# Kernel tuning notes

Measured on AMD Instinct MI355X. Metric: run time of the kernel, lower is better.

## Reference

```python
import jax, jax.numpy as jnp
import numpy as np

DIM = 96
D_STATE = 16
D_CONV = 4
EXPAND = 2
D_INNER = EXPAND * DIM          # 192
DT_RANK = (DIM + 15) // 16      # 6
B, DD, HH, WW = 2, 20, 20, 20
LN_EPS = 1e-5


def setup_inputs() -> dict:
    key = jax.random.key(0)
    ks = jax.random.split(key, 10)
    s = 0.02
    x = jax.random.normal(ks[0], (B, DIM, DD, HH, WW), jnp.float32)
    principal_vector = jax.random.normal(ks[1], (3,), jnp.float32)
    norm_w = jnp.ones((DIM,), jnp.float32)
    norm_b = jnp.zeros((DIM,), jnp.float32)
    in_proj_w = jax.random.normal(ks[2], (2 * D_INNER, DIM), jnp.float32) * s
    conv_w = jax.random.normal(ks[3], (D_INNER, 1, D_CONV), jnp.float32) * 0.3  # depthwise kernel (OIH)
    conv_b = jnp.zeros((D_INNER,), jnp.float32)
    x_proj_w = jax.random.normal(ks[4], (DT_RANK + 2 * D_STATE, D_INNER), jnp.float32) * s
    dt_proj_w = jax.random.normal(ks[5], (D_INNER, DT_RANK), jnp.float32) * (DT_RANK ** -0.5)
    dt_proj_b = jnp.full((D_INNER,), float(np.log(np.expm1(0.01))), jnp.float32)  # softplus^-1(0.01)
    # S4D-real init: A = [1..d_state] per inner channel
    A_log = jnp.log(jnp.broadcast_to(jnp.arange(1, D_STATE + 1, dtype=jnp.float32), (D_INNER, D_STATE)))
    D_param = jnp.ones((D_INNER,), jnp.float32)
    out_proj_w = jax.random.normal(ks[6], (DIM, D_INNER), jnp.float32) * s
    return {"x": x, "principal_vector": principal_vector, "norm_w": norm_w, "norm_b": norm_b,
            "in_proj_w": in_proj_w, "conv_w": conv_w, "conv_b": conv_b, "x_proj_w": x_proj_w,
            "dt_proj_w": dt_proj_w, "dt_proj_b": dt_proj_b, "A_log": A_log, "D_param": D_param,
            "out_proj_w": out_proj_w}


def _mamba(xn, in_proj_w, conv_w, conv_b, x_proj_w, dt_proj_w, dt_proj_b, A_log, D_param, out_proj_w):
    # xn: (B, N, dim)
    xz = jnp.einsum('bnc,ec->bne', xn, in_proj_w)          # (B,N,2*d_inner), no bias
    xc, z = jnp.split(xz, 2, axis=-1)
    # causal depthwise conv1d over sequence, truncated to length N
    xc_t = xc.transpose(0, 2, 1)                           # (B, d_inner, N)
    xc_t = jax.lax.conv_general_dilated(
        xc_t, conv_w, window_strides=(1,), padding=[(D_CONV - 1, 0)],
        dimension_numbers=('NCH', 'OIH', 'NCH'), feature_group_count=D_INNER)
    xc = jax.nn.silu(xc_t + conv_b[None, :, None]).transpose(0, 2, 1)  # (B,N,d_inner)
    x_dbl = jnp.einsum('bnd,ed->bne', xc, x_proj_w)
    dt, Bm, Cm = jnp.split(x_dbl, [DT_RANK, DT_RANK + D_STATE], axis=-1)
    dt = jax.nn.softplus(jnp.einsum('bnr,dr->bnd', dt, dt_proj_w) + dt_proj_b)  # (B,N,d_inner)
    A = -jnp.exp(A_log)                                    # (d_inner, d_state)
    dA = jnp.exp(dt[..., None] * A)                        # (B,N,d_inner,d_state)
    dBx = dt[..., None] * Bm[:, :, None, :] * xc[..., None]

    def comb(c1, c2):
        a1, b1 = c1
        a2, b2 = c2
        return (a1 * a2, a2 * b1 + b2)

    _, h = jax.lax.associative_scan(comb, (dA, dBx), axis=1)  # h_t = dA_t*h_{t-1}+dBx_t
    y = jnp.einsum('bnds,bns->bnd', h, Cm) + D_param * xc
    y = y * jax.nn.silu(z)
    return jnp.einsum('bnd,cd->bnc', y, out_proj_w)


def reference(x, principal_vector, norm_w, norm_b, in_proj_w, conv_w, conv_b, x_proj_w,
              dt_proj_w, dt_proj_b, A_log, D_param, out_proj_w):
    Bb, C, D_, H_, W_ = x.shape
    N = D_ * H_ * W_
    zz, yy, xx = jnp.meshgrid(jnp.arange(D_), jnp.arange(H_), jnp.arange(W_), indexing='ij')
    coords = jnp.stack([zz, yy, xx], axis=-1).reshape(-1, 3).astype(jnp.float32)
    projections = coords @ principal_vector
    sorted_idx = jnp.argsort(projections)
    inv_idx = jnp.argsort(sorted_idx)                      # inverse permutation for scatter-back
    x_flat = x.reshape(Bb, C, N)[:, :, sorted_idx].transpose(0, 2, 1)  # (B,N,C) in PCA order
    mu = x_flat.mean(axis=-1, keepdims=True)
    var = x_flat.var(axis=-1, keepdims=True)               # biased, as torch LayerNorm
    xn = (x_flat - mu) / jnp.sqrt(var + LN_EPS) * norm_w + norm_b
    y = _mamba(xn, in_proj_w, conv_w, conv_b, x_proj_w, dt_proj_w, dt_proj_b, A_log, D_param, out_proj_w)
    out = y[:, inv_idx, :]                                 # back to raster order
    return out.transpose(0, 2, 1).reshape(Bb, C, D_, H_, W_)
```

## Files before the change

### kernel.cpp

```cpp
#include <hip/hip_runtime.h>
#include <math.h>

#define NB 2
#define NC 96
#define NN 8000
#define DI 192
#define DS 16
#define DTRK 6
#define KCH 320
#define LCH 25

#define OFF_RP   0
#define OFF_XN   64000
#define OFF_XC   (OFF_XN + NB*NN*NC)
#define OFF_Z    (OFF_XC + NB*NN*DI)
#define OFF_XCV  (OFF_Z  + NB*NN*DI)
#define OFF_DT   (OFF_XCV + NB*NN*DI)
#define OFF_BM   (OFF_DT + NB*NN*DI)
#define OFF_CM   (OFF_BM + NB*NN*DS)
#define OFF_CA   (OFF_CM + NB*NN*DS)
#define OFF_CB   (OFF_CA + NB*KCH*DI*DS)
#define OFF_HS   (OFF_CB + NB*KCH*DI*DS)
#define OFF_Y    (OFF_HS + NB*KCH*DI*DS)
#define OFF_YP   (OFF_Y  + NB*NN*DI)

__global__ void k_rank(const float* __restrict__ pv, int* __restrict__ rp) {
    __shared__ float kj[1000];
    int t = threadIdx.x;
    float p0 = pv[0], p1 = pv[1], p2 = pv[2];
    int j0 = blockIdx.y * 1000;
    for (int j = t; j < 1000; j += 256) {
        int idx = j0 + j;
        int zz = idx / 400, rem = idx % 400, yy = rem / 20, xx = rem % 20;
        kj[j] = (float)zz * p0 + (float)yy * p1 + (float)xx * p2;
    }
    __syncthreads();
    int i = blockIdx.x * 256 + t;
    if (i >= NN) return;
    {
        int zz = i / 400, rem = i % 400, yy = rem / 20, xx = rem % 20;
        float ki = (float)zz * p0 + (float)yy * p1 + (float)xx * p2;
        int cnt = 0;
        #pragma unroll 4
        for (int j = 0; j < 1000; ++j) {
            float kv = kj[j];
            int jj = j0 + j;
            cnt += (kv < ki || (kv == ki && jj < i)) ? 1 : 0;
        }
        rp[blockIdx.y * 8000 + i] = cnt;
    }
}

__launch_bounds__(256)
__global__ void k_ln(const float* __restrict__ x, const float* __restrict__ nw,
                     const float* __restrict__ nbp, const int* __restrict__ rp,
                     float* __restrict__ xn) {
    __shared__ float xt[64][100];
    __shared__ int rk[64];
    __shared__ float nwb[NC], nbb[NC];
    int b = blockIdx.y, n0 = blockIdx.x * 64, t = threadIdx.x;
    int lane = t & 63, w = t >> 6;
    if (t < 64) {
        int s = 0;
        #pragma unroll
        for (int c = 0; c < 8; ++c) s += rp[c * 8000 + n0 + t];
        rk[t] = s;
    } else if (t >= 64 && t < 160) { int c = t - 64; nwb[c] = nw[c]; nbb[c] = nbp[c]; }
    for (int idx = t; idx < NC * 64; idx += 256) {
        int c = idx >> 6, p = idx & 63;
        xt[p][c] = x[((size_t)b * NC + c) * NN + n0 + p];
    }
    __syncthreads();
    float xr[96];
    float s = 0.f, sq = 0.f;
    #pragma unroll
    for (int c4 = 0; c4 < 24; ++c4) {
        float4 v = *(const float4*)&xt[lane][c4 * 4];
        xr[c4*4+0] = v.x; xr[c4*4+1] = v.y; xr[c4*4+2] = v.z; xr[c4*4+3] = v.w;
        s += v.x + v.y + v.z + v.w;
        sq += v.x*v.x + v.y*v.y + v.z*v.z + v.w*v.w;
    }
    float mu = s * (1.f / 96.f);
    float var = sq * (1.f / 96.f) - mu * mu;
    float rs = rsqrtf(var + 1e-5f);
    #pragma unroll
    for (int c = 0; c < 96; ++c) xr[c] = (xr[c] - mu) * rs * nwb[c] + nbb[c];
    __syncthreads();
    if (w == 0) {
        #pragma unroll
        for (int c = 0; c < 96; ++c) xt[lane][c] = xr[c];
    }
    __syncthreads();
    for (int idx = t; idx < 64 * 24; idx += 256) {
        int p = idx / 24, c4 = idx % 24;
        *(float4*)&xn[((size_t)b * NN + rk[p]) * NC + c4 * 4] = *(const float4*)&xt[p][c4 * 4];
    }
}

__launch_bounds__(256, 3)
__global__ void k_inproj(const float* __restrict__ xn, const float* __restrict__ win,
                         float* __restrict__ xcout, float* __restrict__ zout) {
    __shared__ float wsm[48][100];
    __shared__ float xs[64][100];
    int b = blockIdx.z, g = blockIdx.y, n0 = blockIdx.x * 64, t = threadIdx.x;

    for (int i = t; i < 48 * 24; i += 256) {
        int r = i / 24, c4 = i % 24;
        *(float4*)&wsm[r][c4 * 4] = *(const float4*)(win + (size_t)(g * 48 + r) * NC + c4 * 4);
    }
    for (int i = t; i < 64 * 24; i += 256) {
        int p = i / 24, c4 = i % 24;
        *(float4*)&xs[p][c4 * 4] = *(const float4*)(xn + ((size_t)b * NN + n0 + p) * NC + c4 * 4);
    }
    __syncthreads();

    int oi = t & 15, pi = t >> 4;
    float acc[3][4];
    #pragma unroll
    for (int j = 0; j < 3; ++j)
        #pragma unroll
        for (int pp = 0; pp < 4; ++pp) acc[j][pp] = 0.f;

    for (int c4 = 0; c4 < 24; ++c4) {
        float4 b0 = *(const float4*)&wsm[oi * 3 + 0][c4 * 4];
        float4 b1 = *(const float4*)&wsm[oi * 3 + 1][c4 * 4];
        float4 b2 = *(const float4*)&wsm[oi * 3 + 2][c4 * 4];
        #pragma unroll
        for (int pp = 0; pp < 4; ++pp) {
            float4 a = *(const float4*)&xs[pi * 4 + pp][c4 * 4];
            acc[0][pp] = fmaf(a.x, b0.x, fmaf(a.y, b0.y, fmaf(a.z, b0.z, fmaf(a.w, b0.w, acc[0][pp]))));
            acc[1][pp] = fmaf(a.x, b1.x, fmaf(a.y, b1.y, fmaf(a.z, b1.z, fmaf(a.w, b1.w, acc[1][pp]))));
            acc[2][pp] = fmaf(a.x, b2.x, fmaf(a.y, b2.y, fmaf(a.z, b2.z, fmaf(a.w, b2.w, acc[2][pp]))));
        }
    }
    __syncthreads();
    #pragma unroll
    for (int j = 0; j < 3; ++j)
        #pragma unroll
        for (int pp = 0; pp < 4; ++pp) xs[pi * 4 + pp][oi * 3 + j] = acc[j][pp];
    __syncthreads();

    float* outp = (g < 4) ? xcout : zout;
    int co = (g & 3) * 48;
    for (int i = t; i < 64 * 12; i += 256) {
        int p = i / 12, o4 = i % 12;
        *(float4*)&outp[((size_t)b * NN + n0 + p) * DI + co + o4 * 4] = *(const float4*)&xs[p][o4 * 4];
    }
}

__launch_bounds__(256, 8)
__global__ void k_conv_xdt(const float* __restrict__ cw, const float* __restrict__ cb,
                           const float* __restrict__ xpw, const float* __restrict__ dpw,
                           const float* __restrict__ dpb, const float* __restrict__ xcin,
                           float* __restrict__ xcvout, float* __restrict__ dtout,
                           float* __restrict__ bmout, float* __restrict__ cmout) {
    __shared__ float xcv[8][196];
    __shared__ float dtrT[DTRK][9];
    __shared__ float bc[8][33];
    __shared__ float cwT[4][DI];
    __shared__ float dpwT[DTRK][DI];
    __shared__ float cbl[DI], dpbl[DI];
    int b = blockIdx.y, n0 = blockIdx.x * 8, t = threadIdx.x;
    int l = t & 63, w = t >> 6;
    int p = l & 7, q = l >> 3;

    if (t < DI) {
        cbl[t] = cb[t];
        dpbl[t] = dpb[t];
        #pragma unroll
        for (int k = 0; k < 4; ++k) cwT[k][t] = cw[t * 4 + k];
        #pragma unroll
        for (int r = 0; r < DTRK; ++r) dpwT[r][t] = dpw[t * DTRK + r];
    }
    __syncthreads();

    {
        int pp = t / DI, d = t - pp * DI;
        #pragma unroll
        for (int i = 0; i < 6; ++i) {
            float s = cbl[d];
            #pragma unroll
            for (int k = 0; k < 4; ++k) {
                int n = n0 + pp - 3 + k;
                float xv = (n >= 0) ? xcin[((size_t)b * NN + n) * DI + d] : 0.f;
                s = fmaf(cwT[k][d], xv, s);
            }
            s = s * __builtin_amdgcn_rcpf(1.f + __expf(-s));
            xcv[pp][d] = s;
            xcvout[((size_t)b * NN + n0 + pp) * DI + d] = s;
            pp += 1; d += 64;
            if (d >= DI) { d -= DI; pp += 1; }
        }
    }
    __syncthreads();

    float acc[10];
    #pragma unroll
    for (int j = 0; j < 10; ++j) acc[j] = 0.f;
    #pragma unroll
    for (int ci = 0; ci < 6; ++ci) {
        int c4 = q * 6 + ci;
        float4 xv = *(const float4*)&xcv[p][c4 * 4];
        #pragma unroll
        for (int j = 0; j < 10; ++j) {
            int e = w + 4 * j;
            if (e < 38) {
                float4 w4 = *(const float4*)&xpw[(size_t)e * DI + c4 * 4];
                acc[j] = fmaf(xv.x, w4.x, fmaf(xv.y, w4.y, fmaf(xv.z, w4.z, fmaf(xv.w, w4.w, acc[j]))));
            }
        }
    }
    #pragma unroll
    for (int j = 0; j < 10; ++j) {
        acc[j] += __shfl_xor(acc[j], 8);
        acc[j] += __shfl_xor(acc[j], 16);
        acc[j] += __shfl_xor(acc[j], 32);
    }
    if (l < 8) {
        #pragma unroll
        for (int j = 0; j < 10; ++j) {
            int e = w + 4 * j;
            if (e < DTRK) dtrT[e][p] = acc[j];
            else if (e < 38) bc[p][e - DTRK] = acc[j];
        }
    }
    __syncthreads();

    if (t < 8 * DS) {
        int pp = t >> 4, si = t & 15;
        int n = b * NN + n0 + pp;
        bmout[(size_t)n * DS + si] = bc[pp][si];
        cmout[(size_t)n * DS + si] = bc[pp][DS + si];
    }

    float dv[6];
    {
        int d0 = q * 24 + w * 6;
        #pragma unroll
        for (int jd = 0; jd < 6; ++jd) {
            int d = d0 + jd;
            float v = dpbl[d];
            #pragma unroll
            for (int r = 0; r < DTRK; ++r) v = fmaf(dpwT[r][d], dtrT[r][p], v);
            v = (v > 20.f) ? v : __logf(1.f + __expf(v));
            dv[jd] = v;
        }
    }
    __syncthreads();
    {
        int d0 = q * 24 + w * 6;
        #pragma unroll
        for (int jd = 0; jd < 6; ++jd) xcv[p][d0 + jd] = dv[jd];
    }
    __syncthreads();
    for (int idx = t; idx < 8 * 48; idx += 256) {
        int pp = idx / 48, o4 = idx % 48;
        *(float4*)&dtout[((size_t)b * NN + n0 + pp) * DI + o4 * 4] = *(const float4*)&xcv[pp][o4 * 4];
    }
}

__launch_bounds__(256)
__global__ void k_scan1(const float* __restrict__ alog, const float* __restrict__ dt,
                        const float* __restrict__ xcv, const float* __restrict__ bm,
                        float* __restrict__ ca, float* __restrict__ cbv) {
    int t = threadIdx.x, w = t >> 6, l = t & 63;
    int T = blockIdx.x * 4 + w;
    int b = T / (KCH * 6), rem = T % (KCH * 6);
    int kc = rem / 6, dg = rem % 6;
    int dl = l & 31, sh = l >> 5;
    int d = dg * 32 + dl;
    float a[8];
    #pragma unroll
    for (int j = 0; j < 8; ++j) a[j] = -expf(alog[d * DS + sh * 8 + j]);
    size_t nbase = (size_t)b * NN + kc * LCH;
    float ap[8], hb[8];
    #pragma unroll
    for (int j = 0; j < 8; ++j) { ap[j] = 1.f; hb[j] = 0.f; }
    for (int i = 0; i < LCH; ++i) {
        size_t g = (nbase + i) * DI + d;
        float dtv = dt[g];
        float xv  = xcv[g];
        const float4* b4 = (const float4*)&bm[(nbase + i) * DS + sh * 8];
        float4 b0 = b4[0], b1 = b4[1];
        float bmv[8] = {b0.x,b0.y,b0.z,b0.w,b1.x,b1.y,b1.z,b1.w};
        float bx_ = dtv * xv;
        #pragma unroll
        for (int j = 0; j < 8; ++j) {
            float dA = __expf(dtv * a[j]);
            ap[j] *= dA;
            hb[j] = fmaf(dA, hb[j], bx_ * bmv[j]);
        }
    }
    size_t cidx = ((size_t)(b * KCH + kc) * DI + d) * DS + sh * 8;
    *(float4*)&ca[cidx]      = make_float4(ap[0],ap[1],ap[2],ap[3]);
    *(float4*)&ca[cidx + 4]  = make_float4(ap[4],ap[5],ap[6],ap[7]);
    *(float4*)&cbv[cidx]     = make_float4(hb[0],hb[1],hb[2],hb[3]);
    *(float4*)&cbv[cidx + 4] = make_float4(hb[4],hb[5],hb[6],hb[7]);
}

__global__ void k_scan2(const float* __restrict__ ca, const float* __restrict__ cbv,
                        float* __restrict__ hs) {
    int tid = blockIdx.x * 64 + threadIdx.x;
    int b = tid / (DI * DS), ds_ = tid % (DI * DS);
    size_t base = (size_t)b * KCH * (DI * DS) + ds_;
    float h = 0.f;
    for (int kc = 0; kc < KCH; kc += 8) {
        float av[8], bv[8];
        #pragma unroll
        for (int u = 0; u < 8; ++u) {
            size_t idx = base + (size_t)(kc + u) * (DI * DS);
            av[u] = ca[idx];
            bv[u] = cbv[idx];
        }
        #pragma unroll
        for (int u = 0; u < 8; ++u) {
            hs[base + (size_t)(kc + u) * (DI * DS)] = h;
            h = fmaf(av[u], h, bv[u]);
        }
    }
}

__launch_bounds__(256)
__global__ void k_scan3(const float* __restrict__ alog, const float* __restrict__ Dp,
                        const float* __restrict__ dt, const float* __restrict__ xcv,
                        const float* __restrict__ bm, const float* __restrict__ cm,
                        const float* __restrict__ zin, const float* __restrict__ hs,
                        float* __restrict__ yout) {
    int t = threadIdx.x, w = t >> 6, l = t & 63;
    int T = blockIdx.x * 4 + w;
    int b = T / (KCH * 6), rem = T % (KCH * 6);
    int kc = rem / 6, dg = rem % 6;
    int dl = l & 31, sh = l >> 5;
    int d = dg * 32 + dl;
    float a[8];
    #pragma unroll
    for (int j = 0; j < 8; ++j) a[j] = -expf(alog[d * DS + sh * 8 + j]);
    float dpar = Dp[d];
    size_t nbase = (size_t)b * NN + kc * LCH;
    size_t cidx = ((size_t)(b * KCH + kc) * DI + d) * DS + sh * 8;
    float h[8];
    {
        float4 h0 = *(const float4*)&hs[cidx];
        float4 h1 = *(const float4*)&hs[cidx + 4];
        h[0]=h0.x; h[1]=h0.y; h[2]=h0.z; h[3]=h0.w;
        h[4]=h1.x; h[5]=h1.y; h[6]=h1.z; h[7]=h1.w;
    }
    for (int i = 0; i < LCH; ++i) {
        size_t g = (nbase + i) * DI + d;
        float dtv = dt[g];
        float xv  = xcv[g];
        float zv  = zin[g];
        size_t sb = (nbase + i) * DS + sh * 8;
        const float4* b4 = (const float4*)&bm[sb];
        const float4* c4p = (const float4*)&cm[sb];
        float4 b0 = b4[0], b1 = b4[1];
        float4 c0 = c4p[0], c1 = c4p[1];
        float bmv[8] = {b0.x,b0.y,b0.z,b0.w,b1.x,b1.y,b1.z,b1.w};
        float cmv[8] = {c0.x,c0.y,c0.z,c0.w,c1.x,c1.y,c1.z,c1.w};
        float bx_ = dtv * xv;
        float py = 0.f;
        #pragma unroll
        for (int j = 0; j < 8; ++j) {
            float dA = __expf(dtv * a[j]);
            h[j] = fmaf(dA, h[j], bx_ * bmv[j]);
            py = fmaf(h[j], cmv[j], py);
        }
        py += __shfl_xor(py, 32);
        if (l < 32) {
            float y = py + dpar * xv;
            y *= zv / (1.f + __expf(-zv));
            yout[g] = y;
        }
    }
}

__launch_bounds__(256, 2)
__global__ void k_outproj(const float* __restrict__ ow, const float* __restrict__ yin,
                          float* __restrict__ yp) {
    __shared__ float wsm[32][196];
    __shared__ float yt[64][196];
    int b = blockIdx.z, g = blockIdx.y, n0 = blockIdx.x * 64, t = threadIdx.x;

    for (int i = t; i < 32 * 48; i += 256) {
        int r = i / 48, c4 = i % 48;
        *(float4*)&wsm[r][c4 * 4] = *(const float4*)(ow + (size_t)(g * 32 + r) * DI + c4 * 4);
    }
    for (int i = t; i < 64 * 48; i += 256) {
        int p = i / 48, c4 = i % 48;
        *(float4*)&yt[p][c4 * 4] = *(const float4*)(yin + ((size_t)b * NN + n0 + p) * DI + c4 * 4);
    }
    __syncthreads();

    int l = t & 63, w = t >> 6;
    int oi = l & 7;
    int kq = (l >> 3) & 3;
    int pi = w * 2 + (l >> 5);
    float acc[4][8];
    #pragma unroll
    for (int j = 0; j < 4; ++j)
        #pragma unroll
        for (int pp = 0; pp < 8; ++pp) acc[j][pp] = 0.f;

    for (int c4 = 0; c4 < 12; ++c4) {
        int cg2 = kq * 12 + c4;
        float4 b0 = *(const float4*)&wsm[oi * 4 + 0][cg2 * 4];
        float4 b1 = *(const float4*)&wsm[oi * 4 + 1][cg2 * 4];
        float4 b2 = *(const float4*)&wsm[oi * 4 + 2][cg2 * 4];
        float4 b3 = *(const float4*)&wsm[oi * 4 + 3][cg2 * 4];
        #pragma unroll
        for (int pp = 0; pp < 8; ++pp) {
            float4 a = *(const float4*)&yt[pi * 8 + pp][cg2 * 4];
            acc[0][pp] = fmaf(a.x, b0.x, fmaf(a.y, b0.y, fmaf(a.z, b0.z, fmaf(a.w, b0.w, acc[0][pp]))));
            acc[1][pp] = fmaf(a.x, b1.x, fmaf(a.y, b1.y, fmaf(a.z, b1.z, fmaf(a.w, b1.w, acc[1][pp]))));
            acc[2][pp] = fmaf(a.x, b2.x, fmaf(a.y, b2.y, fmaf(a.z, b2.z, fmaf(a.w, b2.w, acc[2][pp]))));
            acc[3][pp] = fmaf(a.x, b3.x, fmaf(a.y, b3.y, fmaf(a.z, b3.z, fmaf(a.w, b3.w, acc[3][pp]))));
        }
    }
    #pragma unroll
    for (int j = 0; j < 4; ++j)
        #pragma unroll
        for (int pp = 0; pp < 8; ++pp) {
            acc[j][pp] += __shfl_xor(acc[j][pp], 8);
            acc[j][pp] += __shfl_xor(acc[j][pp], 16);
        }
    if (kq == 0) {
        #pragma unroll
        for (int pp = 0; pp < 8; ++pp) {
            float4 v = make_float4(acc[0][pp], acc[1][pp], acc[2][pp], acc[3][pp]);
            *(float4*)&yp[((size_t)b * NN + n0 + pi * 8 + pp) * NC + g * 32 + oi * 4] = v;
        }
    }
}

__launch_bounds__(256)
__global__ void k_final(const float* __restrict__ yp, const int* __restrict__ rp,
                        float* __restrict__ out) {
    __shared__ float ft[64][97];
    __shared__ int rk[64];
    int b = blockIdx.y, i0 = blockIdx.x * 64, t = threadIdx.x;
    if (t < 64) {
        int s = 0;
        #pragma unroll
        for (int c = 0; c < 8; ++c) s += rp[c * 8000 + i0 + t];
        rk[t] = s;
    }
    __syncthreads();
    for (int idx = t; idx < 64 * 24; idx += 256) {
        int ii = idx / 24, j = idx % 24;
        float4 v = *(const float4*)&yp[((size_t)b * NN + rk[ii]) * NC + j * 4];
        ft[ii][j * 4 + 0] = v.x; ft[ii][j * 4 + 1] = v.y;
        ft[ii][j * 4 + 2] = v.z; ft[ii][j * 4 + 3] = v.w;
    }
    __syncthreads();
    for (int idx = t; idx < 96 * 64; idx += 256) {
        int c = idx >> 6, ii = idx & 63;
        out[((size_t)b * NC + c) * NN + i0 + ii] = ft[ii][c];
    }
}

extern "C" void kernel_launch(void* const* d_in, const int* in_sizes, int n_in,
                              void* d_out, int out_size, void* d_ws, size_t ws_size,
                              hipStream_t stream) {
    const float* x    = (const float*)d_in[0];
    const float* pv   = (const float*)d_in[1];
    const float* nw   = (const float*)d_in[2];
    const float* nbp  = (const float*)d_in[3];
    const float* win  = (const float*)d_in[4];
    const float* cw   = (const float*)d_in[5];
    const float* cb   = (const float*)d_in[6];
    const float* xpw  = (const float*)d_in[7];
    const float* dpw  = (const float*)d_in[8];
    const float* dpb  = (const float*)d_in[9];
    const float* alog = (const float*)d_in[10];
    const float* Dp   = (const float*)d_in[11];
    const float* ow   = (const float*)d_in[12];
    float* out = (float*)d_out;
    float* ws  = (float*)d_ws;

    int*   rp   = (int*)ws + OFF_RP;
    float* xn   = ws + OFF_XN;
    float* xc   = ws + OFF_XC;
    float* z    = ws + OFF_Z;
    float* xcv  = ws + OFF_XCV;
    float* dt   = ws + OFF_DT;
    float* bmb  = ws + OFF_BM;
    float* cmb  = ws + OFF_CM;
    float* ca   = ws + OFF_CA;
    float* cbv  = ws + OFF_CB;
    float* hs   = ws + OFF_HS;
    float* y    = ws + OFF_Y;
    float* yp   = ws + OFF_YP;

    k_rank<<<dim3(32, 8), 256, 0, stream>>>(pv, rp);
    k_ln<<<dim3(125, 2), 256, 0, stream>>>(x, nw, nbp, rp, xn);
    k_inproj<<<dim3(125, 8, 2), 256, 0, stream>>>(xn, win, xc, z);
    k_conv_xdt<<<dim3(1000, 2), 256, 0, stream>>>(cw, cb, xpw, dpw, dpb, xc, xcv, dt, bmb, cmb);
    k_scan1<<<(NB * KCH * 6) / 4, 256, 0, stream>>>(alog, dt, xcv, bmb, ca, cbv);
    k_scan2<<<96, 64, 0, stream>>>(ca, cbv, hs);
    k_scan3<<<(NB * KCH * 6) / 4, 256, 0, stream>>>(alog, Dp, dt, xcv, bmb, cmb, z, hs, y);
    k_outproj<<<dim3(125, 3, 2), 256, 0, stream>>>(ow, y, yp);
    k_final<<<dim3(125, 2), 256, 0, stream>>>(yp, rp, out);
}
```

Baseline: 182.9 us.

## Fuse conv/x_proj/dt_proj with chunk-local scan pass into one kernel

```diff
diff --git a/kernel.cpp b/kernel.cpp
--- a/kernel.cpp
+++ b/kernel.cpp
@@ -148,21 +148,23 @@
     }
 }
 
-__launch_bounds__(256, 8)
-__global__ void k_conv_xdt(const float* __restrict__ cw, const float* __restrict__ cb,
-                           const float* __restrict__ xpw, const float* __restrict__ dpw,
-                           const float* __restrict__ dpb, const float* __restrict__ xcin,
-                           float* __restrict__ xcvout, float* __restrict__ dtout,
-                           float* __restrict__ bmout, float* __restrict__ cmout) {
-    __shared__ float xcv[8][196];
-    __shared__ float dtrT[DTRK][9];
-    __shared__ float bc[8][33];
+__launch_bounds__(256, 3)
+__global__ void k_conv_scan1(const float* __restrict__ cw, const float* __restrict__ cb,
+                             const float* __restrict__ xpw, const float* __restrict__ dpw,
+                             const float* __restrict__ dpb, const float* __restrict__ alog,
+                             const float* __restrict__ xcin,
+                             float* __restrict__ xcvout, float* __restrict__ dtout,
+                             float* __restrict__ bmout, float* __restrict__ cmout,
+                             float* __restrict__ ca, float* __restrict__ cbv) {
+    __shared__ float xcv[LCH][196];
+    __shared__ float dts[LCH][DI];
+    __shared__ float bc[LCH][33];
+    __shared__ float dtrT[DTRK][28];
     __shared__ float cwT[4][DI];
     __shared__ float dpwT[DTRK][DI];
     __shared__ float cbl[DI], dpbl[DI];
-    int b = blockIdx.y, n0 = blockIdx.x * 8, t = threadIdx.x;
+    int b = blockIdx.y, kc = blockIdx.x, n0 = kc * LCH, t = threadIdx.x;
     int l = t & 63, w = t >> 6;
-    int p = l & 7, q = l >> 3;
 
     if (t < DI) {
         cbl[t] = cb[t];
@@ -174,128 +176,98 @@
     }
     __syncthreads();
 
+    for (int idx = t; idx < LCH * DI; idx += 256) {
+        int pp = idx / DI, d = idx - pp * DI;
+        float s = cbl[d];
+        #pragma unroll
+        for (int k = 0; k < 4; ++k) {
+            int n = n0 + pp - 3 + k;
+            float xv = (n >= 0) ? xcin[((size_t)b * NN + n) * DI + d] : 0.f;
+            s = fmaf(cwT[k][d], xv, s);
+        }
+        s = s * __builtin_amdgcn_rcpf(1.f + __expf(-s));
+        xcv[pp][d] = s;
+        xcvout[((size_t)b * NN + n0 + pp) * DI + d] = s;
+    }
+    __syncthreads();
+
     {
-        int pp = t / DI, d = t - pp * DI;
-        #pragma unroll
-        for (int i = 0; i < 6; ++i) {
-            float s = cbl[d];
+        int p = (l & 31) < 25 ? (l & 31) : 24;
+        int kh = l >> 5;
+        float acc[10];
+        #pragma unroll
+        for (int j = 0; j < 10; ++j) acc[j] = 0.f;
+        #pragma unroll
+        for (int ci = 0; ci < 24; ++ci) {
+            int c4 = kh * 24 + ci;
+            float4 xv = *(const float4*)&xcv[p][c4 * 4];
             #pragma unroll
-            for (int k = 0; k < 4; ++k) {
-                int n = n0 + pp - 3 + k;
-                float xv = (n >= 0) ? xcin[((size_t)b * NN + n) * DI + d] : 0.f;
-                s = fmaf(cwT[k][d], xv, s);
+            for (int j = 0; j < 10; ++j) {
+                int e = w + 4 * j;
+                if (e < 38) {
+                    float4 w4 = *(const float4*)&xpw[(size_t)e * DI + c4 * 4];
+                    acc[j] = fmaf(xv.x, w4.x, fmaf(xv.y, w4.y, fmaf(xv.z, w4.z, fmaf(xv.w, w4.w, acc[j]))));
+                }
             }
-            s = s * __builtin_amdgcn_rcpf(1.f + __expf(-s));
-            xcv[pp][d] = s;
-            xcvout[((size_t)b * NN + n0 + pp) * DI + d] = s;
-            pp += 1; d += 64;
-            if (d >= DI) { d -= DI; pp += 1; }
-        }
-    }
-    __syncthreads();
-
-    float acc[10];
-    #pragma unroll
-    for (int j = 0; j < 10; ++j) acc[j] = 0.f;
-    #pragma unroll
-    for (int ci = 0; ci < 6; ++ci) {
-        int c4 = q * 6 + ci;
-        float4 xv = *(const float4*)&xcv[p][c4 * 4];
-        #pragma unroll
-        for (int j = 0; j < 10; ++j) {
-            int e = w + 4 * j;
-            if (e < 38) {
-                float4 w4 = *(const float4*)&xpw[(size_t)e * DI + c4 * 4];
-                acc[j] = fmaf(xv.x, w4.x, fmaf(xv.y, w4.y, fmaf(xv.z, w4.z, fmaf(xv.w, w4.w, acc[j]))));
+        }
+        #pragma unroll
+        for (int j = 0; j < 10; ++j) acc[j] += __shfl_xor(acc[j], 32);
+        if ((l & 31) < 25 && l < 32) {
+            #pragma unroll
+            for (int j = 0; j < 10; ++j) {
+                int e = w + 4 * j;
+                if (e < DTRK) dtrT[e][p] = acc[j];
+                else if (e < 38) bc[p][e - DTRK] = acc[j];
             }
         }
     }
-    #pragma unroll
-    for (int j = 0; j < 10; ++j) {
-        acc[j] += __shfl_xor(acc[j], 8);
-        acc[j] += __shfl_xor(acc[j], 16);
-        acc[j] += __shfl_xor(acc[j], 32);
-    }
-    if (l < 8) {
-        #pragma unroll
-        for (int j = 0; j < 10; ++j) {
-            int e = w + 4 * j;
-            if (e < DTRK) dtrT[e][p] = acc[j];
-            else if (e < 38) bc[p][e - DTRK] = acc[j];
-        }
-    }
-    __syncthreads();
-
-    if (t < 8 * DS) {
-        int pp = t >> 4, si = t & 15;
+    __syncthreads();
+
+    for (int idx = t; idx < LCH * DS; idx += 256) {
+        int pp = idx / DS, si = idx % DS;
         int n = b * NN + n0 + pp;
         bmout[(size_t)n * DS + si] = bc[pp][si];
         cmout[(size_t)n * DS + si] = bc[pp][DS + si];
     }
 
-    float dv[6];
+    for (int idx = t; idx < LCH * DI; idx += 256) {
+        int pp = idx / DI, d = idx - pp * DI;
+        float v = dpbl[d];
+        #pragma unroll
+        for (int r = 0; r < DTRK; ++r) v = fmaf(dpwT[r][d], dtrT[r][pp], v);
+        v = (v > 20.f) ? v : __logf(1.f + __expf(v));
+        dts[pp][d] = v;
+        dtout[((size_t)b * NN + n0 + pp) * DI + d] = v;
+    }
+    __syncthreads();
+
     {
-        int d0 = q * 24 + w * 6;
-        #pragma unroll
-        for (int jd = 0; jd < 6; ++jd) {
-            int d = d0 + jd;
-            float v = dpbl[d];
+        float a_[12], ap[12], hb[12];
+        #pragma unroll
+        for (int k = 0; k < 12; ++k) {
+            a_[k] = -expf(alog[t + k * 256]);
+            ap[k] = 1.f; hb[k] = 0.f;
+        }
+        int s_ = t & 15;
+        for (int i = 0; i < LCH; ++i) {
+            float bmv = bc[i][s_];
             #pragma unroll
-            for (int r = 0; r < DTRK; ++r) v = fmaf(dpwT[r][d], dtrT[r][p], v);
-            v = (v > 20.f) ? v : __logf(1.f + __expf(v));
-            dv[jd] = v;
-        }
-    }
-    __syncthreads();
-    {
-        int d0 = q * 24 + w * 6;
-        #pragma unroll
-        for (int jd = 0; jd < 6; ++jd) xcv[p][d0 + jd] = dv[jd];
-    }
-    __syncthreads();
-    for (int idx = t; idx < 8 * 48; idx += 256) {
-        int pp = idx / 48, o4 = idx % 48;
-        *(float4*)&dtout[((size_t)b * NN + n0 + pp) * DI + o4 * 4] = *(const float4*)&xcv[pp][o4 * 4];
-    }
-}
-
-__launch_bounds__(256)
-__global__ void k_scan1(const float* __restrict__ alog, const float* __restrict__ dt,
-                        const float* __restrict__ xcv, const float* __restrict__ bm,
-                        float* __restrict__ ca, float* __restrict__ cbv) {
-    int t = threadIdx.x, w = t >> 6, l = t & 63;
-    int T = blockIdx.x * 4 + w;
-    int b = T / (KCH * 6), rem = T % (KCH * 6);
-    int kc = rem / 6, dg = rem % 6;
-    int dl = l & 31, sh = l >> 5;
-    int d = dg * 32 + dl;
-    float a[8];
-    #pragma unroll
-    for (int j = 0; j < 8; ++j) a[j] = -expf(alog[d * DS + sh * 8 + j]);
-    size_t nbase = (size_t)b * NN + kc * LCH;
-    float ap[8], hb[8];
-    #pragma unroll
-    for (int j = 0; j < 8; ++j) { ap[j] = 1.f; hb[j] = 0.f; }
-    for (int i = 0; i < LCH; ++i) {
-        size_t g = (nbase + i) * DI + d;
-        float dtv = dt[g];
-        float xv  = xcv[g];
-        const float4* b4 = (const float4*)&bm[(nbase + i) * DS + sh * 8];
-        float4 b0 = b4[0], b1 = b4[1];
-        float bmv[8] = {b0.x,b0.y,b0.z,b0.w,b1.x,b1.y,b1.z,b1.w};
-        float bx_ = dtv * xv;
-        #pragma unroll
-        for (int j = 0; j < 8; ++j) {
-            float dA = __expf(dtv * a[j]);
-            ap[j] *= dA;
-            hb[j] = fmaf(dA, hb[j], bx_ * bmv[j]);
-        }
-    }
-    size_t cidx = ((size_t)(b * KCH + kc) * DI + d) * DS + sh * 8;
-    *(float4*)&ca[cidx]      = make_float4(ap[0],ap[1],ap[2],ap[3]);
-    *(float4*)&ca[cidx + 4]  = make_float4(ap[4],ap[5],ap[6],ap[7]);
-    *(float4*)&cbv[cidx]     = make_float4(hb[0],hb[1],hb[2],hb[3]);
-    *(float4*)&cbv[cidx + 4] = make_float4(hb[4],hb[5],hb[6],hb[7]);
+            for (int k = 0; k < 12; ++k) {
+                int d = (t + k * 256) >> 4;
+                float dtv = dts[i][d];
+                float xv  = xcv[i][d];
+                float dA = __expf(dtv * a_[k]);
+                ap[k] *= dA;
+                hb[k] = fmaf(dA, hb[k], dtv * xv * bmv);
+            }
+        }
+        size_t cbase = ((size_t)(b * KCH + kc)) * (DI * DS);
+        #pragma unroll
+        for (int k = 0; k < 12; ++k) {
+            ca [cbase + t + k * 256] = ap[k];
+            cbv[cbase + t + k * 256] = hb[k];
+        }
+    }
 }
 
 __global__ void k_scan2(const float* __restrict__ ca, const float* __restrict__ cbv,
@@ -494,8 +466,8 @@
     k_rank<<<dim3(32, 8), 256, 0, stream>>>(pv, rp);
     k_ln<<<dim3(125, 2), 256, 0, stream>>>(x, nw, nbp, rp, xn);
     k_inproj<<<dim3(125, 8, 2), 256, 0, stream>>>(xn, win, xc, z);
-    k_conv_xdt<<<dim3(1000, 2), 256, 0, stream>>>(cw, cb, xpw, dpw, dpb, xc, xcv, dt, bmb, cmb);
-    k_scan1<<<(NB * KCH * 6) / 4, 256, 0, stream>>>(alog, dt, xcv, bmb, ca, cbv);
+    k_conv_scan1<<<dim3(KCH, 2), 256, 0, stream>>>(cw, cb, xpw, dpw, dpb, alog, xc,
+                                                   xcv, dt, bmb, cmb, ca, cbv);
     k_scan2<<<96, 64, 0, stream>>>(ca, cbv, hs);
     k_scan3<<<(NB * KCH * 6) / 4, 256, 0, stream>>>(alog, Dp, dt, xcv, bmb, cmb, z, hs, y);
     k_outproj<<<dim3(125, 3, 2), 256, 0, stream>>>(ow, y, yp);
```

New measurement: 196.0 us. 1.07x slower.
